# Optimization experiments

Hardware: AMD Instinct MI355X
Metric: run time of the kernel (lower is better)

Reference implementation:

```python
import jax, jax.numpy as jnp
import numpy as np

B, M, D = 2, 8192, 2
N = (64, 64)


def setup_inputs() -> dict:
    key = jax.random.key(0)
    k1, k2 = jax.random.split(key)
    # non-uniform sample points in [-0.5, 0.5)^D
    x = jax.random.uniform(k1, (B, M, D), dtype=jnp.float32) - 0.5
    f_hat = jax.random.normal(k2, (B,) + N, dtype=jnp.float32)
    return {"x": x, "f_hat": f_hat}


def reference(x, f_hat):
    # frequency index grid: cartesian product of arange(-Ni//2, Ni//2) -> [K, D]
    Ns = f_hat.shape[1:]
    grids = [jnp.arange(-(n // 2), n - n // 2, dtype=x.dtype) for n in Ns]
    inds = jnp.stack(jnp.meshgrid(*grids, indexing="ij"), axis=-1).reshape(-1, len(Ns))  # [K, D]
    # phase[b, m, k] = <inds[k], x[b, m]>
    phase = jnp.einsum("bmd,kd->bmk", x, inds)
    fourier = jnp.exp(-2j * jnp.pi * phase)  # [B, M, K] complex64 (the huge intermediate)
    fh = f_hat.reshape(f_hat.shape[0], -1).astype(fourier.dtype)  # [B, K]
    y = jnp.einsum("bmk,bk->bm", fourier, fh)  # [B, M] complex64
    return y
```

## Files before the change

kernel.cpp:

```cpp
#include <hip/hip_runtime.h>
#include <math.h>


#define TWO_PI 6.28318530717958647692f
#define BM 16384

__global__ __launch_bounds__(256) void ndft_kernel(
    const float* __restrict__ x,
    const float* __restrict__ f_hat,
    float* __restrict__ out,
    int planar)
{
    __shared__ float fh[64 * 64];
    __shared__ float part[4][64][2];

    const int t   = threadIdx.x;
    const int sub = t >> 6;
    const int lp  = t & 63;
    const int gp  = blockIdx.x * 64 + lp;
    const int b   = gp >> 13;

    {
        const float4* src = (const float4*)(f_hat + b * 4096);
        float4* dst = (float4*)fh;
        #pragma unroll
        for (int i = 0; i < 4; ++i)
            dst[t + i * 256] = src[t + i * 256];
    }
    __syncthreads();

    const float2 xp = ((const float2*)x)[gp];
    const float x1 = xp.x, x2 = xp.y;

    float s2, c2;
    sincosf(TWO_PI * x2, &s2, &c2);
    float w20i, w20r;
    sincosf(32.0f * TWO_PI * x2, &w20i, &w20r);

    float yr = 0.0f, yi = 0.0f;
    const int k1base = sub << 4;

    for (int k1i = 0; k1i < 16; ++k1i) {
        const int k1 = k1base + k1i;
        float w1i_, w1r_;
        sincosf(-TWO_PI * (float)(k1 - 32) * x1, &w1i_, &w1r_);

        float wr = w20r, wi = w20i;
        float ir = 0.0f, ii = 0.0f;
        const float4* frow = (const float4*)(fh + (k1 << 6));
        #pragma unroll
        for (int q = 0; q < 16; ++q) {
            const float4 f = frow[q];
            {
                ir = fmaf(f.x, wr, ir); ii = fmaf(f.x, wi, ii);
                const float nr = fmaf(wr, c2,  wi * s2);
                const float ni = fmaf(wi, c2, -wr * s2);
                wr = nr; wi = ni;
            }
            {
                ir = fmaf(f.y, wr, ir); ii = fmaf(f.y, wi, ii);
                const float nr = fmaf(wr, c2,  wi * s2);
                const float ni = fmaf(wi, c2, -wr * s2);
                wr = nr; wi = ni;
            }
            {
                ir = fmaf(f.z, wr, ir); ii = fmaf(f.z, wi, ii);
                const float nr = fmaf(wr, c2,  wi * s2);
                const float ni = fmaf(wi, c2, -wr * s2);
                wr = nr; wi = ni;
            }
            {
                ir = fmaf(f.w, wr, ir); ii = fmaf(f.w, wi, ii);
                const float nr = fmaf(wr, c2,  wi * s2);
                const float ni = fmaf(wi, c2, -wr * s2);
                wr = nr; wi = ni;
            }
        }
        yr = fmaf(w1r_, ir, fmaf(-w1i_, ii, yr));
        yi = fmaf(w1r_, ii, fmaf( w1i_, ir, yi));
    }

    part[sub][lp][0] = yr;
    part[sub][lp][1] = yi;
    __syncthreads();

    if (t < 128) {
        const int p = t >> 1, comp = t & 1;
        const float s = part[0][p][comp] + part[1][p][comp]
                      + part[2][p][comp] + part[3][p][comp];
        const int g = blockIdx.x * 64 + p;
        if (planar) {
            out[comp * BM + g] = s;
        } else if (comp == 0) {
            out[g] = s;
        }
    }
}

extern "C" void kernel_launch(void* const* d_in, const int* in_sizes, int n_in,
                              void* d_out, int out_size, void* d_ws, size_t ws_size,
                              hipStream_t stream) {
    const float* x     = (const float*)d_in[0];
    const float* f_hat = (const float*)d_in[1];
    float* out = (float*)d_out;

    const int planar = (out_size >= 2 * BM) ? 1 : 0;

    ndft_kernel<<<dim3(256), dim3(256), 0, stream>>>(x, f_hat, out, planar);
}
```

Baseline: 62.88 us.

## Use Horner evaluation for inner sum, twiddle recurrence, and 512-thread blocks

The inner 64-term sum is now evaluated by Horner's rule on the complex twiddle, folding each coefficient into the recurrence. That cuts the per-term work from about six FMA-type ops to four. The per-row sincos is replaced by a rotating outer-phase recurrence, leaving three sincos per thread instead of seventeen. The block grows to 512 threads with 8 k1 rows each, which doubles the waves per CU and halves the serial chain per thread. Recurrences over many steps may slightly increase rounding error, and the final reduction now sums 8 partials.

```diff
diff --git a/kernel.cpp b/kernel.cpp
--- a/kernel.cpp
+++ b/kernel.cpp
@@ -5,14 +5,14 @@
 #define TWO_PI 6.28318530717958647692f
 #define BM 16384
 
-__global__ __launch_bounds__(256) void ndft_kernel(
+__global__ __launch_bounds__(512) void ndft_kernel(
     const float* __restrict__ x,
     const float* __restrict__ f_hat,
     float* __restrict__ out,
     int planar)
 {
     __shared__ float fh[64 * 64];
-    __shared__ float part[4][64][2];
+    __shared__ float part[8][64][2];
 
     const int t   = threadIdx.x;
     const int sub = t >> 6;
@@ -23,9 +23,8 @@
     {
         const float4* src = (const float4*)(f_hat + b * 4096);
         float4* dst = (float4*)fh;
-        #pragma unroll
-        for (int i = 0; i < 4; ++i)
-            dst[t + i * 256] = src[t + i * 256];
+        dst[t]       = src[t];
+        dst[t + 512] = src[t + 512];
     }
     __syncthreads();
 
@@ -34,50 +33,57 @@
 
     float s2, c2;
     sincosf(TWO_PI * x2, &s2, &c2);
-    float w20i, w20r;
-    sincosf(32.0f * TWO_PI * x2, &w20i, &w20r);
+    const float wr2 = c2, wi2 = -s2;
+
+    float s1, c1;
+    sincosf(TWO_PI * x1, &s1, &c1);
+
+    const int k1base = sub << 3;
+    float Pr, Pi;
+    {
+        const float theta = fmaf(-TWO_PI * (float)(k1base - 32), x1,
+                                 (32.0f * TWO_PI) * x2);
+        sincosf(theta, &Pi, &Pr);
+    }
 
     float yr = 0.0f, yi = 0.0f;
-    const int k1base = sub << 4;
 
-    for (int k1i = 0; k1i < 16; ++k1i) {
+    for (int k1i = 0; k1i < 8; ++k1i) {
         const int k1 = k1base + k1i;
-        float w1i_, w1r_;
-        sincosf(-TWO_PI * (float)(k1 - 32) * x1, &w1i_, &w1r_);
+        const float4* frow = (const float4*)(fh + (k1 << 6));
 
-        float wr = w20r, wi = w20i;
-        float ir = 0.0f, ii = 0.0f;
-        const float4* frow = (const float4*)(fh + (k1 << 6));
+        float Sr = 0.0f, Si = 0.0f;
         #pragma unroll
-        for (int q = 0; q < 16; ++q) {
+        for (int q = 15; q >= 0; --q) {
             const float4 f = frow[q];
             {
-                ir = fmaf(f.x, wr, ir); ii = fmaf(f.x, wi, ii);
-                const float nr = fmaf(wr, c2,  wi * s2);
-                const float ni = fmaf(wi, c2, -wr * s2);
-                wr = nr; wi = ni;
+                const float nr = fmaf(wr2, Sr, fmaf(-wi2, Si, f.w));
+                const float ni = fmaf(wr2, Si, wi2 * Sr);
+                Sr = nr; Si = ni;
             }
             {
-                ir = fmaf(f.y, wr, ir); ii = fmaf(f.y, wi, ii);
-                const float nr = fmaf(wr, c2,  wi * s2);
-                const float ni = fmaf(wi, c2, -wr * s2);
-                wr = nr; wi = ni;
+                const float nr = fmaf(wr2, Sr, fmaf(-wi2, Si, f.z));
+                const float ni = fmaf(wr2, Si, wi2 * Sr);
+                Sr = nr; Si = ni;
             }
             {
-                ir = fmaf(f.z, wr, ir); ii = fmaf(f.z, wi, ii);
-                const float nr = fmaf(wr, c2,  wi * s2);
-                const float ni = fmaf(wi, c2, -wr * s2);
-                wr = nr; wi = ni;
+                const float nr = fmaf(wr2, Sr, fmaf(-wi2, Si, f.y));
+                const float ni = fmaf(wr2, Si, wi2 * Sr);
+                Sr = nr; Si = ni;
             }
             {
-                ir = fmaf(f.w, wr, ir); ii = fmaf(f.w, wi, ii);
-                const float nr = fmaf(wr, c2,  wi * s2);
-                const float ni = fmaf(wi, c2, -wr * s2);
-                wr = nr; wi = ni;
+                const float nr = fmaf(wr2, Sr, fmaf(-wi2, Si, f.x));
+                const float ni = fmaf(wr2, Si, wi2 * Sr);
+                Sr = nr; Si = ni;
             }
         }
-        yr = fmaf(w1r_, ir, fmaf(-w1i_, ii, yr));
-        yi = fmaf(w1r_, ii, fmaf( w1i_, ir, yi));
+
+        yr = fmaf(Pr, Sr, fmaf(-Pi, Si, yr));
+        yi = fmaf(Pr, Si, fmaf( Pi, Sr, yi));
+
+        const float nPr = fmaf(Pr, c1,  Pi * s1);
+        const float nPi = fmaf(Pi, c1, -Pr * s1);
+        Pr = nPr; Pi = nPi;
     }
 
     part[sub][lp][0] = yr;
@@ -86,8 +92,9 @@
 
     if (t < 128) {
         const int p = t >> 1, comp = t & 1;
-        const float s = part[0][p][comp] + part[1][p][comp]
-                      + part[2][p][comp] + part[3][p][comp];
+        float s = 0.0f;
+        #pragma unroll
+        for (int w = 0; w < 8; ++w) s += part[w][p][comp];
         const int g = blockIdx.x * 64 + p;
         if (planar) {
             out[comp * BM + g] = s;
@@ -106,5 +113,5 @@
 
     const int planar = (out_size >= 2 * BM) ? 1 : 0;
 
-    ndft_kernel<<<dim3(256), dim3(256), 0, stream>>>(x, f_hat, out, planar);
+    ndft_kernel<<<dim3(256), dim3(512), 0, stream>>>(x, f_hat, out, planar);
 }
```

Result: no change. 62.16 us (-1.2%).
